# Performance work log

Measured on AMD Instinct MI355X. Metric: run time of the kernel, lower is better.

## Reference

```python
import jax, jax.numpy as jnp
import numpy as np


def gcn_conv(x, src, dst, W, b, num_nodes):
    # GCNConv: add self loops, sym-normalize by deg^{-1/2} on both ends.
    h = x @ W  # [N, out]
    loop = jnp.arange(num_nodes, dtype=src.dtype)
    s = jnp.concatenate([src, loop])
    d = jnp.concatenate([dst, loop])
    deg = jax.ops.segment_sum(jnp.ones(d.shape[0], dtype=h.dtype), d, num_segments=num_nodes)
    dinv = jax.lax.rsqrt(jnp.maximum(deg, 1.0))
    norm = dinv[s] * dinv[d]  # [E+N]
    out = jax.ops.segment_sum(h[s] * norm[:, None], d, num_segments=num_nodes)
    return out + b


def setup_inputs() -> dict:
    key = jax.random.key(0)
    ks = jax.random.split(key, 12)
    N, F, E, ED = 100000, 256, 1600000, 1000000
    x = jax.random.normal(ks[0], (N, F), jnp.float32)
    edge_index = jax.random.randint(ks[1], (2, E), 0, N, jnp.int32)
    total_edges = jax.random.randint(ks[2], (ED, 2), 0, N, jnp.int32)
    PI = jax.random.uniform(ks[3], (ED, 25), jnp.float32)
    W1 = jax.random.normal(ks[4], (F, 100), jnp.float32) * 0.05
    b1 = jnp.zeros((100,), jnp.float32)
    W2 = jax.random.normal(ks[5], (100, 16), jnp.float32) * 0.05
    b2 = jnp.zeros((16,), jnp.float32)
    lin1_W = jax.random.normal(ks[6], (41, 25), jnp.float32) * 0.05
    lin1_b = jnp.zeros((25,), jnp.float32)
    lin_W = jax.random.normal(ks[7], (25, 1), jnp.float32) * 0.05
    lin_b = jnp.zeros((1,), jnp.float32)
    return dict(x=x, edge_index=edge_index, total_edges=total_edges, PI=PI,
                W1=W1, b1=b1, W2=W2, b2=b2,
                lin1_W=lin1_W, lin1_b=lin1_b, lin_W=lin_W, lin_b=lin_b)


def reference(x, edge_index, total_edges, PI, W1, b1, W2, b2, lin1_W, lin1_b, lin_W, lin_b):
    N = x.shape[0]
    src, dst = edge_index[0], edge_index[1]
    # encode (eval mode: dropout is identity)
    h = jax.nn.relu(gcn_conv(x, src, dst, W1, b1, N))
    emb = jax.nn.relu(gcn_conv(h, src, dst, W2, b2, N))
    # renorm_(2, 0, 1): clamp each row's L2 norm to max 1
    nrm = jnp.linalg.norm(emb, axis=1, keepdims=True)
    emb = emb / jnp.maximum(nrm, 1.0)
    # decode: gather endpoint embeddings, squared diff, concat PI, small MLP
    emb_in = emb[total_edges[:, 0]]   # [ED, 16]
    emb_out = emb[total_edges[:, 1]]  # [ED, 16]
    sqdist = (emb_in - emb_out) ** 2  # [ED, 16]
    feat = jnp.concatenate([sqdist, PI], axis=1)  # [ED, 41]
    feat = jax.nn.leaky_relu(feat @ lin1_W + lin1_b, negative_slope=0.2)
    s = jnp.abs(feat @ lin_W + lin_b)[:, 0]
    s = jnp.clip(s, 0.0, 40.0)
    prob = jax.nn.sigmoid(2.0 - s)  # == 1/(exp(s-2)+1)
    return prob
```

## Files before the change

kernel.cpp:

```cpp
#include <hip/hip_runtime.h>
#include <hip/hip_bf16.h>
#include <math.h>

#define H1 100
#define H2 16
#define FDIM 256
#define NPAD 112
#define BINCH 4096

typedef __attribute__((ext_vector_type(8))) short bf16x8;
typedef __attribute__((ext_vector_type(4))) float f32x4;

__device__ __forceinline__ float bf_lo(unsigned u) { return __uint_as_float(u << 16); }
__device__ __forceinline__ float bf_hi(unsigned u) { return __uint_as_float(u & 0xffff0000u); }
__device__ __forceinline__ unsigned f2bf_bits(float f) {
  unsigned x = __float_as_uint(f);
  return (x + 0x7fffu + ((x >> 16) & 1u)) >> 16;
}
__device__ __forceinline__ unsigned pack_bf16(float a, float b) {
  return f2bf_bits(a) | (f2bf_bits(b) << 16);
}


__global__ __launch_bounds__(256)
void k_bincnt(const int* __restrict__ dst, int* __restrict__ bucket_cnt,
              int E, int shift) {
  __shared__ int lcnt[512];
  int t = threadIdx.x;
  for (int i = t; i < 512; i += 256) lcnt[i] = 0;
  __syncthreads();
  int base = blockIdx.x * BINCH;
#pragma unroll
  for (int i = 0; i < 16; i++) {
    int e = base + t + i * 256;
    if (e < E) atomicAdd(&lcnt[dst[e] >> shift], 1);
  }
  __syncthreads();
  for (int b = t; b < 512; b += 256) {
    int c = lcnt[b];
    if (c > 0) atomicAdd(&bucket_cnt[b], c);
  }
}

__global__ void k_bscan(const int* __restrict__ bucket_cnt, int* __restrict__ bucket_base,
                        int* __restrict__ bucket_fill, int nbuc, int E) {
  __shared__ int s[512];
  int tid = threadIdx.x;
  int v = (tid < nbuc) ? bucket_cnt[tid] : 0;
  s[tid] = v;
  __syncthreads();
  for (int off = 1; off < 512; off <<= 1) {
    int tt = (tid >= off) ? s[tid - off] : 0;
    __syncthreads();
    s[tid] += tt;
    __syncthreads();
  }
  if (tid < nbuc) { int ex = s[tid] - v; bucket_base[tid] = ex; bucket_fill[tid] = ex; }
  if (tid == 0) bucket_base[nbuc] = E;
}

__global__ __launch_bounds__(256)
void k_binwrite(const int* __restrict__ src, const int* __restrict__ dst,
                int* __restrict__ bucket_fill, int* __restrict__ tsrc,
                int* __restrict__ tdst, int E, int shift) {
  __shared__ int lcnt[512];
  __shared__ int loff[512];
  int t = threadIdx.x;
  for (int i = t; i < 512; i += 256) lcnt[i] = 0;
  __syncthreads();
  int base = blockIdx.x * BINCH;
  int d[16], s_[16];
#pragma unroll
  for (int i = 0; i < 16; i++) {
    int e = base + t + i * 256;
    if (e < E) {
      d[i] = dst[e]; s_[i] = src[e];
      atomicAdd(&lcnt[d[i] >> shift], 1);
    } else d[i] = -1;
  }
  __syncthreads();
  for (int b = t; b < 512; b += 256) {
    int c = lcnt[b];
    loff[b] = (c > 0) ? atomicAdd(&bucket_fill[b], c) : 0;
  }
  __syncthreads();
#pragma unroll
  for (int i = 0; i < 16; i++) {
    if (d[i] >= 0) {
      int p = atomicAdd(&loff[d[i] >> shift], 1);
      tdst[p] = d[i];
      tsrc[p] = s_[i];
    }
  }
}

__global__ __launch_bounds__(256)
void k_deg2(const int* __restrict__ tdst, const int* __restrict__ bucket_base,
            int* __restrict__ deg, float* __restrict__ dinv, int N, int shift) {
  __shared__ int lcnt[1024];
  int b = blockIdx.x, t = threadIdx.x;
  int bs = 1 << shift, mask = bs - 1;
  for (int i = t; i < bs; i += 256) lcnt[i] = 0;
  __syncthreads();
  int r0 = bucket_base[b], r1 = bucket_base[b + 1];
  for (int e = r0 + t; e < r1; e += 256) atomicAdd(&lcnt[tdst[e] & mask], 1);
  __syncthreads();
  for (int i = t; i < bs; i += 256) {
    int node = (b << shift) + i;
    if (node < N) {
      deg[node] = lcnt[i];
      dinv[node] = rsqrtf((float)(lcnt[i] + 1));
    }
  }
}

__global__ __launch_bounds__(256)
void k_csr2(const int* __restrict__ tsrc, const int* __restrict__ tdst,
            const int* __restrict__ bucket_base, const int* __restrict__ row_ptr,
            int* __restrict__ col_src, int N, int shift) {
  __shared__ int lrp[1024];
  __shared__ int lfill[1024];
  int b = blockIdx.x, t = threadIdx.x;
  int bs = 1 << shift, mask = bs - 1;
  for (int i = t; i < bs; i += 256) {
    int node = (b << shift) + i;
    lrp[i] = row_ptr[node < N ? node : N];
    lfill[i] = 0;
  }
  __syncthreads();
  int r0 = bucket_base[b], r1 = bucket_base[b + 1];
  for (int e = r0 + t; e < r1; e += 256) {
    int dl = tdst[e] & mask;
    int p = lrp[dl] + atomicAdd(&lfill[dl], 1);
    col_src[p] = tsrc[e];
  }
}

__global__ void k_scanA(const int* __restrict__ deg, int* __restrict__ row_ptr,
                        int* __restrict__ psum, int n) {
  __shared__ int s[256];
  int tid = threadIdx.x;
  int i = blockIdx.x * 256 + tid;
  int v = (i < n) ? deg[i] : 0;
  s[tid] = v;
  __syncthreads();
  for (int off = 1; off < 256; off <<= 1) {
    int t = (tid >= off) ? s[tid - off] : 0;
    __syncthreads();
    s[tid] += t;
    __syncthreads();
  }
  if (i < n) row_ptr[i] = s[tid] - v;
  if (tid == 255) psum[blockIdx.x] = s[255];
}

__global__ void k_scanB(int* psum, int nb) {
  __shared__ int s[512];
  int tid = threadIdx.x;
  int v = (tid < nb) ? psum[tid] : 0;
  s[tid] = v;
  __syncthreads();
  for (int off = 1; off < 512; off <<= 1) {
    int t = (tid >= off) ? s[tid - off] : 0;
    __syncthreads();
    s[tid] += t;
    __syncthreads();
  }
  if (tid < nb) psum[tid] = s[tid] - v;
}

__global__ void k_scanC(int* row_ptr, const int* __restrict__ psum, int n, int E) {
  int i = blockIdx.x * blockDim.x + threadIdx.x;
  if (i < n) row_ptr[i] += psum[i >> 8];
  if (i == 0) row_ptr[n] = E;
}

__global__ void k_w1cast(const float* __restrict__ W1, unsigned short* __restrict__ W1bf) {
  int i = blockIdx.x * 256 + threadIdx.x;
  if (i >= NPAD * FDIM) return;
  int col = i / FDIM, k = i % FDIM;
  float v = (col < H1) ? W1[k * H1 + col] : 0.f;
  W1bf[i] = (unsigned short)f2bf_bits(v);
}

__global__ __launch_bounds__(256, 3)
void k_gemm1m(const float* __restrict__ x, const unsigned short* __restrict__ W1bf,
              const float* __restrict__ dinv, unsigned short* __restrict__ t1p, int n) {
  int tid = threadIdx.x;
  int lane = tid & 63, w = tid >> 6;
  int lr = lane & 15, lg = lane >> 4;
  int r0 = blockIdx.x * 64 + w * 16;
  int arow = r0 + lr;
  const float* xrow = x + (size_t)(arow < n ? arow : 0) * FDIM;

  float4 va[16];
#pragma unroll
  for (int s = 0; s < 8; ++s) {
    int kb = s * 32 + lg * 8;
    va[2 * s]     = *(const float4*)(xrow + kb);
    va[2 * s + 1] = *(const float4*)(xrow + kb + 4);
  }
  bf16x8 af[8];
#pragma unroll
  for (int s = 0; s < 8; ++s) {
    uint4 au;
    au.x = pack_bf16(va[2 * s].x, va[2 * s].y);
    au.y = pack_bf16(va[2 * s].z, va[2 * s].w);
    au.z = pack_bf16(va[2 * s + 1].x, va[2 * s + 1].y);
    au.w = pack_bf16(va[2 * s + 1].z, va[2 * s + 1].w);
    af[s] = *(bf16x8*)&au;
  }

  f32x4 acc[7];
#pragma unroll
  for (int nt = 0; nt < 7; nt++) acc[nt] = (f32x4){0.f, 0.f, 0.f, 0.f};

#pragma unroll
  for (int s = 0; s < 8; ++s) {
    int kb = s * 32 + lg * 8;
#pragma unroll
    for (int nt = 0; nt < 7; nt++) {
      int col = nt * 16 + lr;
      bf16x8 b = *(const bf16x8*)(W1bf + (size_t)col * FDIM + kb);
      acc[nt] = __builtin_amdgcn_mfma_f32_16x16x32_bf16(af[s], b, acc[nt], 0, 0, 0);
    }
  }

  float dv[4];
  int rbase = r0 + lg * 4;
#pragma unroll
  for (int r = 0; r < 4; r++) dv[r] = (rbase + r < n) ? dinv[rbase + r] : 0.f;
#pragma unroll
  for (int nt = 0; nt < 7; nt++) {
    int col = nt * 16 + lr;
    if (col < H1) {
#pragma unroll
      for (int r = 0; r < 4; r++) {
        int row = rbase + r;
        if (row < n)
          t1p[(size_t)row * H1 + col] = (unsigned short)f2bf_bits(acc[nt][r] * dv[r]);
      }
    }
  }
}

__global__ __launch_bounds__(256)
void k_agg1(const unsigned* __restrict__ t1p, const int* __restrict__ row_ptr,
            const int* __restrict__ col_src, const float* __restrict__ dinv,
            const float* __restrict__ b1, unsigned* __restrict__ h, int n) {
  int wid = (int)((blockIdx.x * (size_t)blockDim.x + threadIdx.x) >> 6);
  if (wid >= n) return;
  int lane = threadIdx.x & 63;
  if (lane >= 50) return;
  int beg = row_ptr[wid], end = row_ptr[wid + 1];
  float a0 = 0.f, a1 = 0.f;
  for (int e = beg; e < end; e += 8) {
    int last = end - 1;
    int i1 = e + 1 < end ? e + 1 : last;
    int i2 = e + 2 < end ? e + 2 : last;
    int i3 = e + 3 < end ? e + 3 : last;
    int i4 = e + 4 < end ? e + 4 : last;
    int i5 = e + 5 < end ? e + 5 : last;
    int i6 = e + 6 < end ? e + 6 : last;
    int i7 = e + 7 < end ? e + 7 : last;
    int s0 = col_src[e],  s1 = col_src[i1], s2 = col_src[i2], s3 = col_src[i3];
    int s4 = col_src[i4], s5 = col_src[i5], s6 = col_src[i6], s7 = col_src[i7];
    unsigned u0 = t1p[(size_t)s0 * 50 + lane];
    unsigned u1 = t1p[(size_t)s1 * 50 + lane];
    unsigned u2 = t1p[(size_t)s2 * 50 + lane];
    unsigned u3 = t1p[(size_t)s3 * 50 + lane];
    unsigned u4 = t1p[(size_t)s4 * 50 + lane];
    unsigned u5 = t1p[(size_t)s5 * 50 + lane];
    unsigned u6 = t1p[(size_t)s6 * 50 + lane];
    unsigned u7 = t1p[(size_t)s7 * 50 + lane];
    a0 += bf_lo(u0); a1 += bf_hi(u0);
    if (e + 1 < end) { a0 += bf_lo(u1); a1 += bf_hi(u1); }
    if (e + 2 < end) { a0 += bf_lo(u2); a1 += bf_hi(u2); }
    if (e + 3 < end) { a0 += bf_lo(u3); a1 += bf_hi(u3); }
    if (e + 4 < end) { a0 += bf_lo(u4); a1 += bf_hi(u4); }
    if (e + 5 < end) { a0 += bf_lo(u5); a1 += bf_hi(u5); }
    if (e + 6 < end) { a0 += bf_lo(u6); a1 += bf_hi(u6); }
    if (e + 7 < end) { a0 += bf_lo(u7); a1 += bf_hi(u7); }
  }
  unsigned su = t1p[(size_t)wid * 50 + lane];
  a0 += bf_lo(su);
  a1 += bf_hi(su);
  float dv = dinv[wid];
  float v0 = fmaxf(dv * a0 + b1[2 * lane], 0.f);
  float v1 = fmaxf(dv * a1 + b1[2 * lane + 1], 0.f);
  h[(size_t)wid * 50 + lane] = pack_bf16(v0, v1);
}

__global__ __launch_bounds__(256)
void k_gemm2(const unsigned* __restrict__ h, const float* __restrict__ W2,
             const float* __restrict__ dinv, unsigned* __restrict__ t2p, int n) {
  __shared__ alignas(16) float w2s[100][16];
  __shared__ float hs[64][101];
  int tid = threadIdx.x;
  int r0 = blockIdx.x * 64;
  for (int idx = tid; idx < H1 * H2; idx += 256) w2s[idx / 16][idx % 16] = W2[idx];
  for (int idx = tid; idx < 64 * 50; idx += 256) {
    int row = idx / 50, u = idx % 50;
    int gr = r0 + row;
    unsigned v = 0;
    if (gr < n) v = h[(size_t)gr * 50 + u];
    hs[row][2 * u + 0] = bf_lo(v);
    hs[row][2 * u + 1] = bf_hi(v);
  }
  __syncthreads();
  int r = tid & 63, cg = tid >> 6;
  float ax = 0.f, ay = 0.f, az = 0.f, aw = 0.f;
#pragma unroll 4
  for (int k = 0; k < H1; ++k) {
    float a = hs[r][k];
    float4 w = *(const float4*)&w2s[k][cg * 4];
    ax += a * w.x; ay += a * w.y; az += a * w.z; aw += a * w.w;
  }
  int gr = r0 + r;
  if (gr < n) {
    float dv = dinv[gr];
    unsigned u0 = pack_bf16(ax * dv, ay * dv);
    unsigned u1 = pack_bf16(az * dv, aw * dv);
    *(uint2*)(t2p + (size_t)gr * 8 + cg * 2) = make_uint2(u0, u1);
  }
}

__global__ __launch_bounds__(256)
void k_agg2(const unsigned* __restrict__ t2p, const int* __restrict__ row_ptr,
            const int* __restrict__ col_src, const float* __restrict__ dinv,
            const float* __restrict__ b2, float* __restrict__ emb, int n) {
  int wid = (int)((blockIdx.x * (size_t)blockDim.x + threadIdx.x) >> 6);
  if (wid >= n) return;
  int lane = threadIdx.x & 63;
  int es = lane >> 3, c = lane & 7;
  int beg = row_ptr[wid], end = row_ptr[wid + 1];
  float a0 = 0.f, a1 = 0.f;
  for (int e = beg + es; e < end; e += 8) {
    int s = col_src[e];
    unsigned u = t2p[(size_t)s * 8 + c];
    a0 += bf_lo(u);
    a1 += bf_hi(u);
  }
  a0 += __shfl_xor(a0, 8, 64);  a1 += __shfl_xor(a1, 8, 64);
  a0 += __shfl_xor(a0, 16, 64); a1 += __shfl_xor(a1, 16, 64);
  a0 += __shfl_xor(a0, 32, 64); a1 += __shfl_xor(a1, 32, 64);
  unsigned su = t2p[(size_t)wid * 8 + c];
  a0 += bf_lo(su);
  a1 += bf_hi(su);
  float dv = dinv[wid];
  float v0 = fmaxf(dv * a0 + b2[2 * c + 0], 0.f);
  float v1 = fmaxf(dv * a1 + b2[2 * c + 1], 0.f);
  float n2 = v0 * v0 + v1 * v1;
  n2 += __shfl_xor(n2, 1, 64);
  n2 += __shfl_xor(n2, 2, 64);
  n2 += __shfl_xor(n2, 4, 64);
  float scale = 1.f / fmaxf(sqrtf(n2), 1.f);
  if (es == 0) {
    *(float2*)(emb + (size_t)wid * H2 + 2 * c) = make_float2(v0 * scale, v1 * scale);
  }
}

__global__ __launch_bounds__(256)
void k_score(const float* __restrict__ emb, const int* __restrict__ te,
             const float* __restrict__ PI, const float* __restrict__ l1W,
             const float* __restrict__ l1b, const float* __restrict__ lW,
             const float* __restrict__ lb, float* __restrict__ out, int ned) {
  __shared__ alignas(16) float wT[25][44];
  __shared__ float sb1[25], sw2[25];
  for (int idx = threadIdx.x; idx < 41 * 25; idx += blockDim.x) {
    int i = idx / 25, j = idx % 25;
    wT[j][i] = l1W[idx];
  }
  for (int idx = threadIdx.x; idx < 25; idx += blockDim.x) {
    sb1[idx] = l1b[idx];
    sw2[idx] = lW[idx];
  }
  __syncthreads();
  int e = blockIdx.x * blockDim.x + threadIdx.x;
  if (e >= ned) return;
  int u = te[2 * e], v = te[2 * e + 1];
  float f[41];
  const float4* eu = (const float4*)(emb + (size_t)u * H2);
  const float4* ev = (const float4*)(emb + (size_t)v * H2);
#pragma unroll
  for (int q = 0; q < 4; q++) {
    float4 a = eu[q], b = ev[q];
    float dx = a.x - b.x, dy = a.y - b.y, dz = a.z - b.z, dw = a.w - b.w;
    f[q * 4 + 0] = dx * dx; f[q * 4 + 1] = dy * dy;
    f[q * 4 + 2] = dz * dz; f[q * 4 + 3] = dw * dw;
  }
  const float* pi = PI + (size_t)e * 25;
#pragma unroll
  for (int i = 0; i < 25; i++) f[16 + i] = pi[i];
  float acc2 = lb[0];
  for (int j = 0; j < 25; j++) {
    float a = sb1[j];
#pragma unroll
    for (int i = 0; i < 41; i++) a += f[i] * wT[j][i];
    a = (a > 0.f) ? a : 0.2f * a;
    acc2 += a * sw2[j];
  }
  float s = fminf(fabsf(acc2), 40.f);
  float z = 2.f - s;
  out[e] = 1.f / (1.f + __expf(-z));
}

extern "C" void kernel_launch(void* const* d_in, const int* in_sizes, int n_in,
                              void* d_out, int out_size, void* d_ws, size_t ws_size,
                              hipStream_t stream) {
  const float* x   = (const float*)d_in[0];
  const int*   ei  = (const int*)d_in[1];
  const int*   te  = (const int*)d_in[2];
  const float* PI  = (const float*)d_in[3];
  const float* W1  = (const float*)d_in[4];
  const float* b1  = (const float*)d_in[5];
  const float* W2  = (const float*)d_in[6];
  const float* b2  = (const float*)d_in[7];
  const float* l1W = (const float*)d_in[8];
  const float* l1b = (const float*)d_in[9];
  const float* lW  = (const float*)d_in[10];
  const float* lb  = (const float*)d_in[11];
  float* out = (float*)d_out;

  int h1 = in_sizes[5];
  int F  = in_sizes[4] / h1;
  int N  = in_sizes[0] / F;
  int E  = in_sizes[1] / 2;
  int ED = in_sizes[2] / 2;

  const int* src  = ei;
  const int* dstp = ei + E;

  int shift = 8;
  while ((((size_t)N + ((size_t)1 << shift) - 1) >> shift) > 512) shift++;
  int nbuc = (N + (1 << shift) - 1) >> shift;

  size_t off = 0;
  auto alloc = [&](size_t bytes) -> void* {
    void* p = (char*)d_ws + off;
    off += (bytes + 255) & ~(size_t)255;
    return p;
  };
  int*            deg      = (int*)alloc((size_t)N * 4);
  float*          dinv     = (float*)alloc((size_t)N * 4);
  int*            row_ptr  = (int*)alloc((size_t)(N + 1) * 4);
  int*            psum     = (int*)alloc(512 * 4);
  int*            bcnt     = (int*)alloc(512 * 4);
  int*            bbase    = (int*)alloc(520 * 4);
  int*            bfill    = (int*)alloc(512 * 4);
  int*            col_src  = (int*)alloc((size_t)E * 4);
  unsigned short* W1bf     = (unsigned short*)alloc((size_t)NPAD * FDIM * 2);
  unsigned*       t1p      = (unsigned*)alloc((size_t)N * 50 * 4);
  unsigned*       h        = (unsigned*)alloc((size_t)N * 50 * 4);
  unsigned*       t2p      = (unsigned*)alloc((size_t)N * 8 * 4);
  float*          emb      = (float*)alloc((size_t)N * H2 * 4);

  int* tdst = (int*)h;
  int* tsrc = (int*)h + E;

  int nb = (N + 255) / 256;
  int nwb = (E + BINCH - 1) / BINCH;

  hipMemsetAsync(bcnt, 0, 512 * 4, stream);
  k_bincnt<<<nwb, 256, 0, stream>>>(dstp, bcnt, E, shift);
  k_bscan<<<1, 512, 0, stream>>>(bcnt, bbase, bfill, nbuc, E);
  k_binwrite<<<nwb, 256, 0, stream>>>(src, dstp, bfill, tsrc, tdst, E, shift);
  k_deg2<<<nbuc, 256, 0, stream>>>(tdst, bbase, deg, dinv, N, shift);
  k_scanA<<<nb, 256, 0, stream>>>(deg, row_ptr, psum, N);
  k_scanB<<<1, 512, 0, stream>>>(psum, nb);
  k_scanC<<<nb, 256, 0, stream>>>(row_ptr, psum, N, E);
  k_csr2<<<nbuc, 256, 0, stream>>>(tsrc, tdst, bbase, row_ptr, col_src, N, shift);
  k_w1cast<<<(NPAD * FDIM + 255) / 256, 256, 0, stream>>>(W1, W1bf);
  k_gemm1m<<<(N + 63) / 64, 256, 0, stream>>>(x, W1bf, dinv, (unsigned short*)t1p, N);
  k_agg1<<<(int)(((size_t)N * 64 + 255) / 256), 256, 0, stream>>>(t1p, row_ptr, col_src, dinv, b1, h, N);
  k_gemm2<<<(N + 63) / 64, 256, 0, stream>>>(h, W2, dinv, t2p, N);
  k_agg2<<<(int)(((size_t)N * 64 + 255) / 256), 256, 0, stream>>>(t2p, row_ptr, col_src, dinv, b2, emb, N);
  k_score<<<(ED + 255) / 256, 256, 0, stream>>>(emb, te, PI, l1W, l1b, lW, lb, out, ED);
}
```

Before: 339.9 us.

## Stage W1 in swizzled LDS for GEMM1 and use MFMA for edge-score MLP

GEMM1 now uses 512-thread blocks that first copy the bf16 W1 tile into XOR-swizzled shared memory, so B fragments are read from LDS rather than from global memory. The edge-scoring kernel is rewritten so each wave handles 16 edges and computes the 41x25 first layer with bf16 MFMA instructions, reducing the second layer with cross-lane shuffles. This replaces roughly a thousand scalar FMAs per edge with matrix instructions. The cost is bf16 rounding of the squared distances and PI features, plus a 56KB LDS allocation per block that may limit occupancy.

After: 317.0 us. 6.8% less time.

```diff
diff --git a/kernel.cpp b/kernel.cpp
--- a/kernel.cpp
+++ b/kernel.cpp
@@ -10,6 +10,7 @@
 
 typedef __attribute__((ext_vector_type(8))) short bf16x8;
 typedef __attribute__((ext_vector_type(4))) float f32x4;
+typedef float f32x4a __attribute__((ext_vector_type(4), aligned(4)));
 
 __device__ __forceinline__ float bf_lo(unsigned u) { return __uint_as_float(u << 16); }
 __device__ __forceinline__ float bf_hi(unsigned u) { return __uint_as_float(u & 0xffff0000u); }
@@ -20,7 +21,6 @@
 __device__ __forceinline__ unsigned pack_bf16(float a, float b) {
   return f2bf_bits(a) | (f2bf_bits(b) << 16);
 }
-
 
 __global__ __launch_bounds__(256)
 void k_bincnt(const int* __restrict__ dst, int* __restrict__ bucket_cnt,
@@ -183,13 +183,14 @@
   W1bf[i] = (unsigned short)f2bf_bits(v);
 }
 
-__global__ __launch_bounds__(256, 3)
+__global__ __launch_bounds__(512, 2)
 void k_gemm1m(const float* __restrict__ x, const unsigned short* __restrict__ W1bf,
               const float* __restrict__ dinv, unsigned short* __restrict__ t1p, int n) {
+  __shared__ unsigned short ws[NPAD * FDIM];
   int tid = threadIdx.x;
   int lane = tid & 63, w = tid >> 6;
   int lr = lane & 15, lg = lane >> 4;
-  int r0 = blockIdx.x * 64 + w * 16;
+  int r0 = blockIdx.x * 128 + w * 16;
   int arow = r0 + lr;
   const float* xrow = x + (size_t)(arow < n ? arow : 0) * FDIM;
 
@@ -200,6 +201,17 @@
     va[2 * s]     = *(const float4*)(xrow + kb);
     va[2 * s + 1] = *(const float4*)(xrow + kb + 4);
   }
+
+  for (int i = tid; i < NPAD * FDIM / 8; i += 512) {
+    int col = i >> 5;
+    int kc = i & 31;
+    uint4 v = *(const uint4*)(W1bf + col * FDIM + kc * 8);
+    unsigned addr = (unsigned)(col * 512 + kc * 16) ^ ((unsigned)(col & 7) << 4);
+    *(uint4*)((char*)ws + addr) = v;
+  }
+  asm volatile("" ::: "memory");
+  __syncthreads();
+
   bf16x8 af[8];
 #pragma unroll
   for (int s = 0; s < 8; ++s) {
@@ -221,7 +233,8 @@
 #pragma unroll
     for (int nt = 0; nt < 7; nt++) {
       int col = nt * 16 + lr;
-      bf16x8 b = *(const bf16x8*)(W1bf + (size_t)col * FDIM + kb);
+      unsigned addr = (unsigned)(col * 512 + kb * 2) ^ ((unsigned)(col & 7) << 4);
+      bf16x8 b = *(bf16x8*)((char*)ws + addr);
       acc[nt] = __builtin_amdgcn_mfma_f32_16x16x32_bf16(af[s], b, acc[nt], 0, 0, 0);
     }
   }
@@ -365,44 +378,114 @@
              const float* __restrict__ PI, const float* __restrict__ l1W,
              const float* __restrict__ l1b, const float* __restrict__ lW,
              const float* __restrict__ lb, float* __restrict__ out, int ned) {
-  __shared__ alignas(16) float wT[25][44];
-  __shared__ float sb1[25], sw2[25];
-  for (int idx = threadIdx.x; idx < 41 * 25; idx += blockDim.x) {
-    int i = idx / 25, j = idx % 25;
-    wT[j][i] = l1W[idx];
-  }
-  for (int idx = threadIdx.x; idx < 25; idx += blockDim.x) {
-    sb1[idx] = l1b[idx];
-    sw2[idx] = lW[idx];
-  }
-  __syncthreads();
-  int e = blockIdx.x * blockDim.x + threadIdx.x;
-  if (e >= ned) return;
-  int u = te[2 * e], v = te[2 * e + 1];
-  float f[41];
-  const float4* eu = (const float4*)(emb + (size_t)u * H2);
-  const float4* ev = (const float4*)(emb + (size_t)v * H2);
-#pragma unroll
-  for (int q = 0; q < 4; q++) {
-    float4 a = eu[q], b = ev[q];
-    float dx = a.x - b.x, dy = a.y - b.y, dz = a.z - b.z, dw = a.w - b.w;
-    f[q * 4 + 0] = dx * dx; f[q * 4 + 1] = dy * dy;
-    f[q * 4 + 2] = dz * dz; f[q * 4 + 3] = dw * dw;
-  }
-  const float* pi = PI + (size_t)e * 25;
-#pragma unroll
-  for (int i = 0; i < 25; i++) f[16 + i] = pi[i];
-  float acc2 = lb[0];
-  for (int j = 0; j < 25; j++) {
-    float a = sb1[j];
-#pragma unroll
-    for (int i = 0; i < 41; i++) a += f[i] * wT[j][i];
-    a = (a > 0.f) ? a : 0.2f * a;
-    acc2 += a * sw2[j];
-  }
-  float s = fminf(fabsf(acc2), 40.f);
-  float z = 2.f - s;
-  out[e] = 1.f / (1.f + __expf(-z));
+  int tid = threadIdx.x;
+  int lane = tid & 63, w = tid >> 6;
+  int lr = lane & 15, lg = lane >> 4;
+  int e0w = blockIdx.x * 64 + w * 16;
+  int e = e0w + lr;
+  int ec = (e < ned) ? e : 0;
+
+  float wb[16];
+#pragma unroll
+  for (int i = 0; i < 8; i++) {
+    int k0 = lg * 8 + i;
+    wb[i] = (lr < 25) ? l1W[k0 * 25 + lr] : 0.f;
+    int k1 = 32 + lg * 8 + i;
+    wb[8 + i] = (lr < 25 && k1 < 41) ? l1W[k1 * 25 + lr] : 0.f;
+  }
+  int j1 = 16 + lr;
+  float wb2[16];
+#pragma unroll
+  for (int i = 0; i < 8; i++) {
+    int k0 = lg * 8 + i;
+    wb2[i] = (j1 < 25) ? l1W[k0 * 25 + j1] : 0.f;
+    int k1 = 32 + lg * 8 + i;
+    wb2[8 + i] = (j1 < 25 && k1 < 41) ? l1W[k1 * 25 + j1] : 0.f;
+  }
+  uint4 B00, B01, B10, B11;
+  B00.x = pack_bf16(wb[0], wb[1]);  B00.y = pack_bf16(wb[2], wb[3]);
+  B00.z = pack_bf16(wb[4], wb[5]);  B00.w = pack_bf16(wb[6], wb[7]);
+  B01.x = pack_bf16(wb[8], wb[9]);  B01.y = pack_bf16(wb[10], wb[11]);
+  B01.z = pack_bf16(wb[12], wb[13]); B01.w = pack_bf16(wb[14], wb[15]);
+  B10.x = pack_bf16(wb2[0], wb2[1]); B10.y = pack_bf16(wb2[2], wb2[3]);
+  B10.z = pack_bf16(wb2[4], wb2[5]); B10.w = pack_bf16(wb2[6], wb2[7]);
+  B11.x = pack_bf16(wb2[8], wb2[9]); B11.y = pack_bf16(wb2[10], wb2[11]);
+  B11.z = pack_bf16(wb2[12], wb2[13]); B11.w = pack_bf16(wb2[14], wb2[15]);
+
+  uint4 A0 = {0u, 0u, 0u, 0u}, A1 = {0u, 0u, 0u, 0u};
+  const float* pie = PI + (size_t)ec * 25;
+  if (lg < 2) {
+    int2 uv = *(const int2*)(te + 2 * (size_t)ec);
+    const float* eu = emb + (size_t)uv.x * H2 + lg * 8;
+    const float* ev = emb + (size_t)uv.y * H2 + lg * 8;
+    float4 a0 = *(const float4*)(eu);
+    float4 a1 = *(const float4*)(eu + 4);
+    float4 b0 = *(const float4*)(ev);
+    float4 b1 = *(const float4*)(ev + 4);
+    float d0 = a0.x - b0.x, d1 = a0.y - b0.y, d2 = a0.z - b0.z, d3 = a0.w - b0.w;
+    float d4 = a1.x - b1.x, d5 = a1.y - b1.y, d6 = a1.z - b1.z, d7 = a1.w - b1.w;
+    A0.x = pack_bf16(d0 * d0, d1 * d1);
+    A0.y = pack_bf16(d2 * d2, d3 * d3);
+    A0.z = pack_bf16(d4 * d4, d5 * d5);
+    A0.w = pack_bf16(d6 * d6, d7 * d7);
+    if (lg == 0) {
+      f32x4a p0 = *(const f32x4a*)(pie + 16);
+      f32x4a p1 = *(const f32x4a*)(pie + 20);
+      A1.x = pack_bf16(p0[0], p0[1]); A1.y = pack_bf16(p0[2], p0[3]);
+      A1.z = pack_bf16(p1[0], p1[1]); A1.w = pack_bf16(p1[2], p1[3]);
+    } else {
+      A1.x = pack_bf16(pie[24], 0.f);
+    }
+  } else if (lg == 2) {
+    f32x4a p0 = *(const f32x4a*)(pie);
+    f32x4a p1 = *(const f32x4a*)(pie + 4);
+    A0.x = pack_bf16(p0[0], p0[1]); A0.y = pack_bf16(p0[2], p0[3]);
+    A0.z = pack_bf16(p1[0], p1[1]); A0.w = pack_bf16(p1[2], p1[3]);
+  } else {
+    f32x4a p0 = *(const f32x4a*)(pie + 8);
+    f32x4a p1 = *(const f32x4a*)(pie + 12);
+    A0.x = pack_bf16(p0[0], p0[1]); A0.y = pack_bf16(p0[2], p0[3]);
+    A0.z = pack_bf16(p1[0], p1[1]); A0.w = pack_bf16(p1[2], p1[3]);
+  }
+
+  f32x4 acc0 = {0.f, 0.f, 0.f, 0.f}, acc1 = {0.f, 0.f, 0.f, 0.f};
+  acc0 = __builtin_amdgcn_mfma_f32_16x16x32_bf16(*(bf16x8*)&A0, *(bf16x8*)&B00, acc0, 0, 0, 0);
+  acc0 = __builtin_amdgcn_mfma_f32_16x16x32_bf16(*(bf16x8*)&A1, *(bf16x8*)&B01, acc0, 0, 0, 0);
+  acc1 = __builtin_amdgcn_mfma_f32_16x16x32_bf16(*(bf16x8*)&A0, *(bf16x8*)&B10, acc1, 0, 0, 0);
+  acc1 = __builtin_amdgcn_mfma_f32_16x16x32_bf16(*(bf16x8*)&A1, *(bf16x8*)&B11, acc1, 0, 0, 0);
+
+  float bj0 = l1b[lr];
+  float wj0 = lW[lr];
+  float bj1 = (j1 < 25) ? l1b[j1] : 0.f;
+  float wj1 = (j1 < 25) ? lW[j1] : 0.f;
+  float lbv = lb[0];
+  float part[4];
+#pragma unroll
+  for (int r = 0; r < 4; r++) {
+    float a0v = acc0[r] + bj0;
+    a0v = (a0v > 0.f) ? a0v : 0.2f * a0v;
+    float a1v = acc1[r] + bj1;
+    a1v = (a1v > 0.f) ? a1v : 0.2f * a1v;
+    part[r] = a0v * wj0 + ((j1 < 25) ? a1v * wj1 : 0.f);
+  }
+#pragma unroll
+  for (int r = 0; r < 4; r++) {
+    part[r] += __shfl_xor(part[r], 1, 64);
+    part[r] += __shfl_xor(part[r], 2, 64);
+    part[r] += __shfl_xor(part[r], 4, 64);
+    part[r] += __shfl_xor(part[r], 8, 64);
+  }
+  if (lr == 0) {
+#pragma unroll
+    for (int r = 0; r < 4; r++) {
+      int eo = e0w + lg * 4 + r;
+      if (eo < ned) {
+        float s = fminf(fabsf(part[r] + lbv), 40.f);
+        float z = 2.f - s;
+        out[eo] = 1.f / (1.f + __expf(-z));
+      }
+    }
+  }
 }
 
 extern "C" void kernel_launch(void* const* d_in, const int* in_sizes, int n_in,
@@ -471,9 +554,9 @@
   k_scanC<<<nb, 256, 0, stream>>>(row_ptr, psum, N, E);
   k_csr2<<<nbuc, 256, 0, stream>>>(tsrc, tdst, bbase, row_ptr, col_src, N, shift);
   k_w1cast<<<(NPAD * FDIM + 255) / 256, 256, 0, stream>>>(W1, W1bf);
-  k_gemm1m<<<(N + 63) / 64, 256, 0, stream>>>(x, W1bf, dinv, (unsigned short*)t1p, N);
+  k_gemm1m<<<(N + 127) / 128, 512, 0, stream>>>(x, W1bf, dinv, (unsigned short*)t1p, N);
   k_agg1<<<(int)(((size_t)N * 64 + 255) / 256), 256, 0, stream>>>(t1p, row_ptr, col_src, dinv, b1, h, N);
   k_gemm2<<<(N + 63) / 64, 256, 0, stream>>>(h, W2, dinv, t2p, N);
   k_agg2<<<(int)(((size_t)N * 64 + 255) / 256), 256, 0, stream>>>(t2p, row_ptr, col_src, dinv, b2, emb, N);
-  k_score<<<(ED + 255) / 256, 256, 0, stream>>>(emb, te, PI, l1W, l1b, lW, lb, out, ED);
-}
+  k_score<<<(ED + 63) / 64, 256, 0, stream>>>(emb, te, PI, l1W, l1b, lW, lb, out, ED);
+}
```
